# Optimization experiments

Hardware: AMD Instinct MI355X
Metric: run time of the kernel (lower is better)

Reference implementation:

```python
import jax, jax.numpy as jnp
import numpy as np

B, T, N, H = 16, 49, 64, 128  # batch, input_window_size-1, nbones, hidden_size


def setup_inputs() -> dict:
    key = jax.random.key(0)
    ks = jax.random.split(key, 13)
    s = 0.1  # keep gate preactivations in a sane range
    inp = {
        "h": jax.random.normal(ks[0], (B, T, N, H), jnp.float32),
        "c_h": jax.random.normal(ks[1], (B, T, N, H), jnp.float32),
        "p": jax.random.normal(ks[2], (B, T, N, H), jnp.float32),
        "g_t": jax.random.normal(ks[3], (B, T, 1, H), jnp.float32),
        "c_g_t": jax.random.normal(ks[4], (B, T, 1, H), jnp.float32),
        # 8 h-update gates stacked: order = (i, f_lt, f_ft, f_rt, f_s, g, o, c)
        "U": jax.random.normal(ks[5], (8, T, H, H), jnp.float32) * s,     # acts on p
        "Wt": jax.random.normal(ks[6], (8, T, 3 * H, H), jnp.float32) * s,  # acts on [h_before,h,h_after]
        "Ws": jax.random.normal(ks[7], (8, T, H, H), jnp.float32) * s,    # acts on h_s_before
        "Zt": jax.random.normal(ks[8], (8, T, H, H), jnp.float32) * s,    # acts on g_t
        "b": jax.random.normal(ks[9], (8, T, 1, H), jnp.float32) * s,
        # 3 g_t-update gates stacked: order = (forget_f, g, o)
        "Wg": jax.random.normal(ks[10], (3, T, H, H), jnp.float32) * s,
        "Zg": jax.random.normal(ks[11], (3, T, H, H), jnp.float32) * s,
        "bg": jax.random.normal(ks[12], (3, T, 1, H), jnp.float32) * s,
        "train": 0,
    }
    return inp


def _forward(h, c_h, p, g_t, c_g_t, U, Wt, Ws, Zt, b, Wg, Zg, bg):
    zt = jnp.zeros_like(h[:, :1])        # temporal padding [B,1,N,H]
    zs = jnp.zeros_like(h[:, :, :1])     # spatial  padding [B,T,1,H]
    h_tb = jnp.concatenate([zt, h[:, :-1]], axis=1)
    h_ta = jnp.concatenate([h[:, 1:], zt], axis=1)
    h_tba = jnp.concatenate([h_tb, h, h_ta], axis=3)   # [B,T,N,3H]
    c_tb = jnp.concatenate([zt, c_h[:, :-1]], axis=1)
    c_ta = jnp.concatenate([c_h[:, 1:], zt], axis=1)
    h_sb = jnp.concatenate([zs, h[:, :, :-1]], axis=2)
    c_sb = jnp.concatenate([zs, c_h[:, :, :-1]], axis=2)

    # all 8 gate preactivations at once; per-timestep weights contracted with einsum
    pre = (jnp.einsum('btnh,gthk->gbtnk', p, U)
           + jnp.einsum('btnd,gtdk->gbtnk', h_tba, Wt)
           + jnp.einsum('btnh,gthk->gbtnk', h_sb, Ws)
           + jnp.einsum('btoh,gthk->gbtok', g_t, Zt)   # o == 1, broadcasts over bones
           + b[:, None])                               # [8,B,T,N,H]
    i_n, f_lt, f_ft, f_rt, f_s, g_n, o_n = jax.nn.sigmoid(pre[:7])
    c_n = jnp.tanh(pre[7])

    c_h_new = (i_n * c_n + f_lt * c_tb + f_ft * c_h + f_rt * c_ta
               + f_s * c_sb + g_n * c_g_t)
    h_new = o_n * jnp.tanh(c_h_new)

    # global (g_t) state update
    h_mean = jnp.mean(h_new, axis=2, keepdims=True)    # [B,T,1,H]
    f_gtf = jax.nn.sigmoid(jnp.einsum('btnh,thk->btnk', h_new, Wg[0])
                           + jnp.einsum('btoh,thk->btok', g_t, Zg[0]) + bg[0])
    g_gtg = jax.nn.sigmoid(jnp.einsum('btoh,thk->btok', h_mean, Wg[1])
                           + jnp.einsum('btoh,thk->btok', g_t, Zg[1]) + bg[1])
    o_gto = jax.nn.sigmoid(jnp.einsum('btoh,thk->btok', h_mean, Wg[2])
                           + jnp.einsum('btoh,thk->btok', g_t, Zg[2]) + bg[2])
    c_g_new = jnp.mean(f_gtf * c_h_new, axis=2, keepdims=True) + g_gtg * c_g_t
    g_new = jnp.tanh(c_g_new) * o_gto
    return h_new, c_h_new, g_new, c_g_new


def reference(h, c_h, p, g_t, c_g_t, U, Wt, Ws, Zt, b, Wg, Zg, bg, train):
    return _forward(h, c_h, p, g_t, c_g_t, U, Wt, Ws, Zt, b, Wg, Zg, bg)
```

## Files before the change

### kernel.cpp

```cpp
#include <hip/hip_runtime.h>
#include <hip/hip_bf16.h>

#define TD 49
#define BD 16
#define ND 64
#define HD 128

typedef float  f32x4  __attribute__((ext_vector_type(4)));
typedef __bf16 bf16x8 __attribute__((ext_vector_type(8)));
typedef __bf16 bf16x4 __attribute__((ext_vector_type(4)));

#define WP_OFF   0u
#define HB_OFF   32112640u
#define ACT_ELEMS 6422528u
#define PB_OFF   38535168u
#define GB_OFF   44957696u
#define GT_ELEMS 100352u
#define ZP_OFF   45058048u
#define ZB_OFF   45060096u

#define OUT_H    0
#define OUT_CH   6422528
#define OUT_G    12845056
#define OUT_CG   12945408

#define KPAD 136
#define LDS1_BYTES 49152
#define LDS2_BYTES 118784

#define NB_ACTS 12644
#define NB_ZB   392
#define NB_W    1960

__device__ __forceinline__ float sigf(float x) {
    return 1.0f / (1.0f + exp2f(-1.442695041f * x));
}
__device__ __forceinline__ float tanhf_fast(float x) {
    x = fminf(fmaxf(x, -20.f), 20.f);
    float e = exp2f(2.885390082f * x);
    return (e - 1.f) / (e + 1.f);
}
__device__ __forceinline__ void gload16(const void* g, void* l) {
    __builtin_amdgcn_global_load_lds((const __attribute__((address_space(1))) void*)g,
                                     (__attribute__((address_space(3))) void*)l, 16, 0, 0);
}

__global__ __launch_bounds__(256) void prep_kernel(
    const float* __restrict__ h, const float* __restrict__ p,
    const float* __restrict__ g, const float* __restrict__ Zt,
    const float* __restrict__ bias, const float* __restrict__ U,
    const float* __restrict__ Wt, const float* __restrict__ Ws,
    __bf16* __restrict__ ws)
{
    __shared__ float gl[16][128];
    const int bid = blockIdx.x;
    const int tid = threadIdx.x;

    if (bid < NB_ACTS) {
        unsigned i = bid * 256u + tid;
        const unsigned HU = ACT_ELEMS / 4u, GU = GT_ELEMS / 4u;
        const float* src;
        unsigned dst;
        if (i < HU)              { src = h + (size_t)i * 4;            dst = HB_OFF + i * 4; }
        else if (i < 2u*HU)      { unsigned j = i - HU;    src = p + (size_t)j * 4; dst = PB_OFF + j * 4; }
        else if (i < 2u*HU + GU) { unsigned j = i - 2u*HU; src = g + (size_t)j * 4; dst = GB_OFF + j * 4; }
        else if (i < 2u*HU + GU + 512u) {
            unsigned j = i - 2u*HU - GU;
            bf16x4 z = {};
            *(bf16x4*)(ws + ZP_OFF + j * 4) = z;
            return;
        } else return;
        f32x4 v = *(const f32x4*)src;
        bf16x4 w;
        w[0] = (__bf16)v[0]; w[1] = (__bf16)v[1]; w[2] = (__bf16)v[2]; w[3] = (__bf16)v[3];
        *(bf16x4*)(ws + dst) = w;
        return;
    }

    if (bid < NB_ACTS + NB_ZB) {
        int zid = bid - NB_ACTS;
        int t = zid >> 3, gg = zid & 7;
#pragma unroll
        for (int j = 0; j < 8; ++j) {
            int idx = j * 256 + tid;
            int b = idx >> 7, k = idx & 127;
            gl[b][k] = g[((b * TD + t) << 7) + k];
        }
        __syncthreads();

        int h_ = tid & 127, bh = tid >> 7;
        float* zbf = (float*)(ws + ZB_OFF);
        float s[8];
        float bv = bias[(gg * TD + t) * HD + h_];
#pragma unroll
        for (int b8 = 0; b8 < 8; ++b8) s[b8] = bv;
        const float* Zrow = Zt + ((size_t)(gg * TD + t) << 14) + h_;
#pragma unroll 4
        for (int k = 0; k < 128; ++k) {
            float zv = Zrow[k << 7];
#pragma unroll
            for (int b8 = 0; b8 < 8; ++b8)
                s[b8] += gl[bh * 8 + b8][k] * zv;
        }
#pragma unroll
        for (int b8 = 0; b8 < 8; ++b8) {
            int bt = (bh * 8 + b8) * TD + t;
            zbf[(bt * 8 + gg) * HD + h_] = s[b8];
        }
        return;
    }

    {
        int wb = bid - NB_ACTS - NB_ZB;
        int tg = wb / 5, kc = wb % 5;
        int t = tg >> 3, gg = tg & 7;
        int gt = gg * TD + t;
        const float* S;
        int kloc0;
        if (kc == 0)      { S = U  + ((size_t)gt << 14); kloc0 = 0; }
        else if (kc <= 3) { S = Wt + (size_t)gt * 49152; kloc0 = (kc - 1) * 128; }
        else              { S = Ws + ((size_t)gt << 14); kloc0 = 0; }
        __bf16* wrow = ws + WP_OFF + (size_t)tg * 81920 + kc * 128;
#pragma unroll
        for (int u = 0; u < 8; ++u) {
            int gid = u * 256 + tid;
            int hh = gid >> 4, kq = gid & 15;
            const float* s = S + (size_t)(kloc0 + kq * 8) * 128 + hh;
            bf16x8 w;
#pragma unroll
            for (int j = 0; j < 8; ++j) w[j] = (__bf16)s[j * 128];
            *(bf16x8*)(wrow + (size_t)hh * 640 + kq * 8) = w;
        }
    }
}

__global__ __launch_bounds__(256, 3) void phase1_kernel(
    const __bf16* __restrict__ ws,
    const float* __restrict__ c_h, const float* __restrict__ c_g_t,
    float* __restrict__ out)
{
    extern __shared__ __bf16 smem[];
    const __bf16* hb = ws + HB_OFF;
    const __bf16* pb = ws + PB_OFF;
    const __bf16* wp = ws + WP_OFF;
    const __bf16* zp = ws + ZP_OFF;
    const float*  zb = (const float*)(ws + ZB_OFF);

    int bid = blockIdx.x;
    int swz = (bid & 7) * 392 + (bid >> 3);
    int t     = swz >> 6;
    int rem   = swz & 63;
    int mtile = rem >> 3, ntile = rem & 7;

    int tid  = threadIdx.x;
    int wave = tid >> 6, lane = tid & 63;
    int lg = lane >> 4, l16 = lane & 15;

    const __bf16* pA[2][5];
    const __bf16* pB[2];
    int dstA[2], dstB[2];
#pragma unroll
    for (int it = 0; it < 2; ++it) {
        int chunk = it * 256 + tid;
        int row   = chunk >> 2;
        int k16   = chunk & 3;
        int ke    = (k16 ^ ((row >> 1) & 3)) * 8;
        int b_ = mtile * 2 + (row >> 6), n_ = row & 63, bt_ = b_ * TD + t;
        pA[it][0] = pb + ((bt_ * ND + n_) << 7) + ke;
        pA[it][1] = (t > 0)      ? hb + (((bt_ - 1) * ND + n_) << 7) + ke : zp + ke;
        pA[it][2] = hb + ((bt_ * ND + n_) << 7) + ke;
        pA[it][3] = (t < TD - 1) ? hb + (((bt_ + 1) * ND + n_) << 7) + ke : zp + ke;
        pA[it][4] = (n_ > 0)     ? hb + ((bt_ * ND + n_ - 1) << 7) + ke : zp + ke;
        int g_ = row >> 4, hc = row & 15;
        pB[it] = wp + (size_t)((t * 8 + g_) * 128 + ntile * 16 + hc) * 640 + ke;
        dstA[it] = chunk * 8;
        dstB[it] = 12288 + chunk * 8;
    }

    int rbA[2], rbB[8];
#pragma unroll
    for (int mi = 0; mi < 2; ++mi) {
        int row = wave * 32 + mi * 16 + l16;
        rbA[mi] = row * 64 + ((lg ^ ((row >> 1) & 3)) << 4);
    }
#pragma unroll
    for (int g = 0; g < 8; ++g) {
        int row = g * 16 + l16;
        rbB[g] = row * 64 + ((lg ^ ((row >> 1) & 3)) << 4);
    }

    f32x4 acc[2][8];
    const f32x4 vzero = {0.f, 0.f, 0.f, 0.f};
#pragma unroll
    for (int mi = 0; mi < 2; ++mi)
#pragma unroll
        for (int g = 0; g < 8; ++g) acc[mi][g] = vzero;

#define STAGE(KS) do {                                                          \
        const int sl = (KS) % 3;                                                \
        _Pragma("unroll")                                                       \
        for (int it = 0; it < 2; ++it) {                                        \
            gload16(pA[it][(KS) >> 2] + ((KS) & 3) * 32,                        \
                    smem + sl * 4096 + dstA[it]);                               \
            gload16(pB[it] + (KS) * 32,                                         \
                    smem + sl * 4096 + dstB[it]);                               \
        }                                                                       \
    } while (0)

    STAGE(0); STAGE(1);
    asm volatile("s_waitcnt vmcnt(4)" ::: "memory");
    __builtin_amdgcn_s_barrier();

#pragma unroll
    for (int ks = 0; ks < 20; ++ks) {
        if (ks + 2 < 20) STAGE(ks + 2);
        const char* Ab = (const char*)smem + (ks % 3) * 8192;
        const char* Bb = (const char*)smem + 24576 + (ks % 3) * 8192;
        bf16x8 af[2], bfr[8];
        af[0] = *(const bf16x8*)(Ab + rbA[0]);
        af[1] = *(const bf16x8*)(Ab + rbA[1]);
#pragma unroll
        for (int g = 0; g < 8; ++g)
            bfr[g] = *(const bf16x8*)(Bb + rbB[g]);
#pragma unroll
        for (int g = 0; g < 8; ++g) {
            acc[0][g] = __builtin_amdgcn_mfma_f32_16x16x32_bf16(af[0], bfr[g], acc[0][g], 0, 0, 0);
            acc[1][g] = __builtin_amdgcn_mfma_f32_16x16x32_bf16(af[1], bfr[g], acc[1][g], 0, 0, 0);
        }
        if (ks < 19) {
            if (ks + 2 < 20) asm volatile("s_waitcnt vmcnt(4)" ::: "memory");
            else             asm volatile("s_waitcnt vmcnt(0)" ::: "memory");
            __builtin_amdgcn_s_barrier();
        }
    }
#undef STAGE

    const int hcol = ntile * 16 + l16;
#pragma unroll
    for (int mi = 0; mi < 2; ++mi) {
#pragma unroll
        for (int r = 0; r < 4; ++r) {
            int RG = mtile * 128 + wave * 32 + mi * 16 + lg * 4 + r;
            int b  = RG >> 6, nn = RG & 63;
            int bt = b * TD + t;
            int base = ((bt * ND + nn) << 7) + hcol;
            const float* zrow = zb + (bt * 8) * HD + hcol;
            float pre[8];
#pragma unroll
            for (int g = 0; g < 8; ++g) pre[g] = acc[mi][g][r] + zrow[g * HD];
            float i_  = sigf(pre[0]);
            float flt = sigf(pre[1]);
            float fft = sigf(pre[2]);
            float frt = sigf(pre[3]);
            float fs  = sigf(pre[4]);
            float gn  = sigf(pre[5]);
            float on  = sigf(pre[6]);
            float cn  = tanhf_fast(pre[7]);
            float ccur = c_h[base];
            float ctb  = (t > 0)      ? c_h[base - ND * HD] : 0.f;
            float cta  = (t < TD - 1) ? c_h[base + ND * HD] : 0.f;
            float csb  = (nn > 0)     ? c_h[base - HD]      : 0.f;
            float cg   = c_g_t[(bt << 7) + hcol];
            float cnew = i_ * cn + flt * ctb + fft * ccur + frt * cta + fs * csb + gn * cg;
            float hnew = on * tanhf_fast(cnew);
            out[OUT_H  + base] = hnew;
            out[OUT_CH + base] = cnew;
        }
    }
}

__global__ __launch_bounds__(256, 1) void phase2_kernel(
    const float* __restrict__ g_t, const float* __restrict__ c_g_t,
    const float* __restrict__ Wg,  const float* __restrict__ Zg,
    const float* __restrict__ bg,  float* __restrict__ out)
{
    extern __shared__ char sm2[];
    __bf16* A2  = (__bf16*)sm2;
    __bf16* Wb  = (__bf16*)(sm2 + 69632);
    float*  gts = (float*)(sm2 + 69632 + 34816);
    float*  hm  = (float*)(sm2 + 69632 + 34816 + 2048);
    float*  dts = (float*)(sm2 + 69632 + 34816 + 4096);

    int bid = blockIdx.x;
    int t = bid >> 2, bq = bid & 3;
    int tid = threadIdx.x;
    int wv = tid >> 6, lane = tid & 63, lg = lane >> 4, l16 = lane & 15;

    const float* hn  = out + OUT_H;
    const float* chn = out + OUT_CH;

#pragma unroll
    for (int j = 0; j < 32; ++j) {
        int fid = j * 256 + tid;
        int r = fid >> 5, k = (fid & 31) << 2;
        int b = bq * 4 + (r >> 6), nn = r & 63, bt = b * TD + t;
        f32x4 v = *(const f32x4*)(hn + ((bt * ND + nn) << 7) + k);
        bf16x4 w;
        w[0] = (__bf16)v[0]; w[1] = (__bf16)v[1]; w[2] = (__bf16)v[2]; w[3] = (__bf16)v[3];
        *(bf16x4*)(A2 + r * KPAD + k) = w;
    }
#pragma unroll
    for (int j = 0; j < 2; ++j) {
        int idx = j * 256 + tid;
        int b4 = idx >> 7, c = idx & 127;
        gts[idx] = g_t[(((bq * 4 + b4) * TD + t) << 7) + c];
    }
    __syncthreads();

#pragma unroll
    for (int j = 0; j < 2; ++j) {
        int idx = j * 256 + tid;
        int b4 = idx >> 7, c = idx & 127;
        float s = 0.f;
        for (int nn = 0; nn < 64; ++nn) s += (float)A2[(b4 * 64 + nn) * KPAD + c];
        hm[idx] = s * (1.f / 64.f);
    }
    __syncthreads();

    for (int m = 0; m < 5; ++m) {
        const float* M = (m < 3) ? (Zg + ((size_t)(m * TD + t) << 14))
                                 : (Wg + ((size_t)((m - 2) * TD + t) << 14));
#pragma unroll
        for (int j = 0; j < 16; ++j) {
            int fid = j * 256 + tid;
            int k = fid >> 5, c4 = (fid & 31) << 2;
            f32x4 v = *(const f32x4*)(M + (k << 7) + c4);
            bf16x4 w;
            w[0] = (__bf16)v[0]; w[1] = (__bf16)v[1]; w[2] = (__bf16)v[2]; w[3] = (__bf16)v[3];
            *(bf16x4*)(Wb + k * KPAD + c4) = w;
        }
        __syncthreads();
        const float* vec = (m >= 3) ? hm : gts;
#pragma unroll
        for (int j = 0; j < 2; ++j) {
            int idx = j * 256 + tid;
            int b4 = idx >> 7, c = idx & 127;
            float s = 0.f;
            for (int k = 0; k < 128; ++k) s += vec[b4 * 128 + k] * (float)Wb[k * KPAD + c];
            dts[(m * 4 + b4) * 128 + c] = s;
        }
        __syncthreads();
    }

    {
        const float* M = Wg + ((size_t)t << 14);
#pragma unroll
        for (int j = 0; j < 16; ++j) {
            int fid = j * 256 + tid;
            int k = fid >> 5, q = fid & 31;
            f32x4 v = *(const f32x4*)(M + (k << 7) + q * 4);
            int cb = q * 4;
            Wb[(cb + 0) * KPAD + k] = (__bf16)v[0];
            Wb[(cb + 1) * KPAD + k] = (__bf16)v[1];
            Wb[(cb + 2) * KPAD + k] = (__bf16)v[2];
            Wb[(cb + 3) * KPAD + k] = (__bf16)v[3];
        }
        __syncthreads();
    }

    f32x4 acc[4][8];
    const f32x4 vzero = {0.f, 0.f, 0.f, 0.f};
#pragma unroll
    for (int mi = 0; mi < 4; ++mi)
#pragma unroll
        for (int ni = 0; ni < 8; ++ni) acc[mi][ni] = vzero;
#pragma unroll
    for (int ks = 0; ks < 4; ++ks) {
        int kb = ks * 32 + lg * 8;
        bf16x8 a[4];
#pragma unroll
        for (int mi = 0; mi < 4; ++mi)
            a[mi] = *(const bf16x8*)(A2 + (wv * 64 + mi * 16 + l16) * KPAD + kb);
#pragma unroll
        for (int ni = 0; ni < 8; ++ni) {
            bf16x8 bfr = *(const bf16x8*)(Wb + (ni * 16 + l16) * KPAD + kb);
#pragma unroll
            for (int mi = 0; mi < 4; ++mi)
                acc[mi][ni] = __builtin_amdgcn_mfma_f32_16x16x32_bf16(a[mi], bfr, acc[mi][ni], 0, 0, 0);
        }
    }

    int b = bq * 4 + wv, bt = b * TD + t;
#pragma unroll
    for (int ni = 0; ni < 8; ++ni) {
        int col = ni * 16 + l16;
        float z = dts[(0 * 4 + wv) * 128 + col] + bg[t * HD + col];
        float macc = 0.f;
#pragma unroll
        for (int mi = 0; mi < 4; ++mi) {
#pragma unroll
            for (int r = 0; r < 4; ++r) {
                int row = mi * 16 + lg * 4 + r;
                float f  = sigf(acc[mi][ni][r] + z);
                float cv = chn[((bt * ND + row) << 7) + col];
                macc += f * cv;
            }
        }
        macc += __shfl_xor(macc, 16, 64);
        macc += __shfl_xor(macc, 32, 64);
        if (lg == 0) {
            float Mn  = macc * (1.f / 64.f);
            float g_g = sigf(dts[(3 * 4 + wv) * 128 + col] + dts[(1 * 4 + wv) * 128 + col]
                             + bg[(TD + t) * HD + col]);
            float o_g = sigf(dts[(4 * 4 + wv) * 128 + col] + dts[(2 * 4 + wv) * 128 + col]
                             + bg[(2 * TD + t) * HD + col]);
            float cgt = c_g_t[(bt << 7) + col];
            float cgn = Mn + g_g * cgt;
            out[OUT_G  + (bt << 7) + col] = tanhf_fast(cgn) * o_g;
            out[OUT_CG + (bt << 7) + col] = cgn;
        }
    }
}

extern "C" void kernel_launch(void* const* d_in, const int* in_sizes, int n_in,
                              void* d_out, int out_size, void* d_ws, size_t ws_size,
                              hipStream_t stream) {
    const float* h     = (const float*)d_in[0];
    const float* c_h   = (const float*)d_in[1];
    const float* p     = (const float*)d_in[2];
    const float* g_t   = (const float*)d_in[3];
    const float* c_g_t = (const float*)d_in[4];
    const float* U     = (const float*)d_in[5];
    const float* Wt    = (const float*)d_in[6];
    const float* Ws    = (const float*)d_in[7];
    const float* Zt    = (const float*)d_in[8];
    const float* b     = (const float*)d_in[9];
    const float* Wg    = (const float*)d_in[10];
    const float* Zg    = (const float*)d_in[11];
    const float* bg    = (const float*)d_in[12];
    float* out = (float*)d_out;
    __bf16* ws = (__bf16*)d_ws;

    prep_kernel<<<NB_ACTS + NB_ZB + NB_W, 256, 0, stream>>>(h, p, g_t, Zt, b, U, Wt, Ws, ws);

    (void)hipFuncSetAttribute(reinterpret_cast<const void*>(phase1_kernel),
                              hipFuncAttributeMaxDynamicSharedMemorySize, LDS1_BYTES);
    (void)hipFuncSetAttribute(reinterpret_cast<const void*>(phase2_kernel),
                              hipFuncAttributeMaxDynamicSharedMemorySize, LDS2_BYTES);
    phase1_kernel<<<TD * 64, 256, LDS1_BYTES, stream>>>(ws, c_h, c_g_t, out);
    phase2_kernel<<<TD * 4, 256, LDS2_BYTES, stream>>>(g_t, c_g_t, Wg, Zg, bg, out);
}
```

Before: 254.3 us.

## Restructure g_t update: precompute Zg terms, fuse h_mean into phase1, widen phase2 grid

```diff
diff --git a/kernel.cpp b/kernel.cpp
--- a/kernel.cpp
+++ b/kernel.cpp
@@ -18,6 +18,9 @@
 #define GT_ELEMS 100352u
 #define ZP_OFF   45058048u
 #define ZB_OFF   45060096u
+#define HM_OFF   46665728u
+#define DTSG_OFF 46866432u
+#define W0P_OFF  47468544u
 
 #define OUT_H    0
 #define OUT_CH   6422528
@@ -26,11 +29,13 @@
 
 #define KPAD 136
 #define LDS1_BYTES 49152
-#define LDS2_BYTES 118784
+#define LDS2_BYTES 73728
 
 #define NB_ACTS 12644
 #define NB_ZB   392
 #define NB_W    1960
+#define NB_DTSG 147
+#define NB_W0   49
 
 __device__ __forceinline__ float sigf(float x) {
     return 1.0f / (1.0f + exp2f(-1.442695041f * x));
@@ -50,7 +55,8 @@
     const float* __restrict__ g, const float* __restrict__ Zt,
     const float* __restrict__ bias, const float* __restrict__ U,
     const float* __restrict__ Wt, const float* __restrict__ Ws,
-    __bf16* __restrict__ ws)
+    const float* __restrict__ Zg, const float* __restrict__ bg,
+    const float* __restrict__ Wg, __bf16* __restrict__ ws)
 {
     __shared__ float gl[16][128];
     const int bid = blockIdx.x;
@@ -87,7 +93,6 @@
             gl[b][k] = g[((b * TD + t) << 7) + k];
         }
         __syncthreads();
-
         int h_ = tid & 127, bh = tid >> 7;
         float* zbf = (float*)(ws + ZB_OFF);
         float s[8];
@@ -110,7 +115,7 @@
         return;
     }
 
-    {
+    if (bid < NB_ACTS + NB_ZB + NB_W) {
         int wb = bid - NB_ACTS - NB_ZB;
         int tg = wb / 5, kc = wb % 5;
         int t = tg >> 3, gg = tg & 7;
@@ -131,13 +136,62 @@
             for (int j = 0; j < 8; ++j) w[j] = (__bf16)s[j * 128];
             *(bf16x8*)(wrow + (size_t)hh * 640 + kq * 8) = w;
         }
+        return;
+    }
+
+    if (bid < NB_ACTS + NB_ZB + NB_W + NB_DTSG) {
+        int zid = bid - NB_ACTS - NB_ZB - NB_W;
+        int t = zid / 3, m = zid % 3;
+#pragma unroll
+        for (int j = 0; j < 8; ++j) {
+            int idx = j * 256 + tid;
+            int b = idx >> 7, k = idx & 127;
+            gl[b][k] = g[((b * TD + t) << 7) + k];
+        }
+        __syncthreads();
+        int h_ = tid & 127, bh = tid >> 7;
+        float* dtf = (float*)(ws + DTSG_OFF);
+        float s[8];
+        float bv = bg[(m * TD + t) * HD + h_];
+#pragma unroll
+        for (int b8 = 0; b8 < 8; ++b8) s[b8] = bv;
+        const float* Zrow = Zg + ((size_t)(m * TD + t) << 14) + h_;
+#pragma unroll 4
+        for (int k = 0; k < 128; ++k) {
+            float zv = Zrow[k << 7];
+#pragma unroll
+            for (int b8 = 0; b8 < 8; ++b8)
+                s[b8] += gl[bh * 8 + b8][k] * zv;
+        }
+#pragma unroll
+        for (int b8 = 0; b8 < 8; ++b8) {
+            int bt = (bh * 8 + b8) * TD + t;
+            dtf[(m * BD * TD + bt) * HD + h_] = s[b8];
+        }
+        return;
+    }
+
+    {
+        int t = bid - NB_ACTS - NB_ZB - NB_W - NB_DTSG;
+        const float* S = Wg + ((size_t)t << 14);
+        __bf16* dst0 = ws + W0P_OFF + (size_t)t * 16384;
+#pragma unroll
+        for (int u = 0; u < 8; ++u) {
+            int gid = u * 256 + tid;
+            int hh = gid >> 4, kq = gid & 15;
+            const float* s = S + (size_t)(kq * 8) * 128 + hh;
+            bf16x8 w;
+#pragma unroll
+            for (int j = 0; j < 8; ++j) w[j] = (__bf16)s[j * 128];
+            *(bf16x8*)(dst0 + (size_t)hh * 128 + kq * 8) = w;
+        }
     }
 }
 
 __global__ __launch_bounds__(256, 3) void phase1_kernel(
     const __bf16* __restrict__ ws,
     const float* __restrict__ c_h, const float* __restrict__ c_g_t,
-    float* __restrict__ out)
+    float* __restrict__ hmf, float* __restrict__ out)
 {
     extern __shared__ __bf16 smem[];
     const __bf16* hb = ws + HB_OFF;
@@ -236,6 +290,7 @@
 #undef STAGE
 
     const int hcol = ntile * 16 + l16;
+    float s_loc = 0.f;
 #pragma unroll
     for (int mi = 0; mi < 2; ++mi) {
 #pragma unroll
@@ -265,150 +320,132 @@
             float hnew = on * tanhf_fast(cnew);
             out[OUT_H  + base] = hnew;
             out[OUT_CH + base] = cnew;
-        }
-    }
-}
-
-__global__ __launch_bounds__(256, 1) void phase2_kernel(
-    const float* __restrict__ g_t, const float* __restrict__ c_g_t,
-    const float* __restrict__ Wg,  const float* __restrict__ Zg,
-    const float* __restrict__ bg,  float* __restrict__ out)
+            s_loc += hnew;
+        }
+    }
+    s_loc += __shfl_xor(s_loc, 16, 64);
+    s_loc += __shfl_xor(s_loc, 32, 64);
+    __syncthreads();
+    float* redf = (float*)smem;
+    if (lane < 16) redf[wave * 16 + lane] = s_loc;
+    __syncthreads();
+    if (tid < 32) {
+        int bsel = tid >> 4, c = tid & 15;
+        float hv = (redf[(bsel * 2) * 16 + c] + redf[(bsel * 2 + 1) * 16 + c]) * (1.f / 64.f);
+        hmf[((mtile * 2 + bsel) * TD + t) * HD + ntile * 16 + c] = hv;
+    }
+}
+
+__global__ __launch_bounds__(256, 2) void phase2_kernel(
+    const __bf16* __restrict__ ws, const float* __restrict__ c_g_t,
+    const float* __restrict__ Wg, float* __restrict__ out)
 {
     extern __shared__ char sm2[];
     __bf16* A2  = (__bf16*)sm2;
-    __bf16* Wb  = (__bf16*)(sm2 + 69632);
-    float*  gts = (float*)(sm2 + 69632 + 34816);
-    float*  hm  = (float*)(sm2 + 69632 + 34816 + 2048);
-    float*  dts = (float*)(sm2 + 69632 + 34816 + 4096);
+    __bf16* Wb  = (__bf16*)(sm2 + 34816);
+    float*  hm2 = (float*)(sm2 + 69632);
+    float*  red = (float*)(sm2 + 70656);
 
     int bid = blockIdx.x;
-    int t = bid >> 2, bq = bid & 3;
+    int swz = (bid & 7) * 49 + (bid >> 3);
+    int t = swz >> 3, mtile = swz & 7;
     int tid = threadIdx.x;
     int wv = tid >> 6, lane = tid & 63, lg = lane >> 4, l16 = lane & 15;
 
-    const float* hn  = out + OUT_H;
-    const float* chn = out + OUT_CH;
-
-#pragma unroll
-    for (int j = 0; j < 32; ++j) {
+    const float* hn   = out + OUT_H;
+    const float* chn  = out + OUT_CH;
+    const float* hmf  = (const float*)(ws + HM_OFF);
+    const float* dtf  = (const float*)(ws + DTSG_OFF);
+    const __bf16* w0p = ws + W0P_OFF + (size_t)t * 16384;
+
+#pragma unroll
+    for (int j = 0; j < 16; ++j) {
         int fid = j * 256 + tid;
         int r = fid >> 5, k = (fid & 31) << 2;
-        int b = bq * 4 + (r >> 6), nn = r & 63, bt = b * TD + t;
+        int b = mtile * 2 + (r >> 6), nn = r & 63, bt = b * TD + t;
         f32x4 v = *(const f32x4*)(hn + ((bt * ND + nn) << 7) + k);
         bf16x4 w;
         w[0] = (__bf16)v[0]; w[1] = (__bf16)v[1]; w[2] = (__bf16)v[2]; w[3] = (__bf16)v[3];
         *(bf16x4*)(A2 + r * KPAD + k) = w;
     }
 #pragma unroll
-    for (int j = 0; j < 2; ++j) {
+    for (int j = 0; j < 8; ++j) {
         int idx = j * 256 + tid;
-        int b4 = idx >> 7, c = idx & 127;
-        gts[idx] = g_t[(((bq * 4 + b4) * TD + t) << 7) + c];
+        int hh = idx >> 4, kq = idx & 15;
+        bf16x8 v = *(const bf16x8*)(w0p + hh * 128 + kq * 8);
+        *(bf16x8*)(Wb + hh * KPAD + kq * 8) = v;
+    }
+    {
+        int b4 = tid >> 7, c = tid & 127;
+        hm2[b4 * 128 + c] = hmf[((mtile * 2 + b4) * TD + t) * HD + c];
     }
     __syncthreads();
 
-#pragma unroll
-    for (int j = 0; j < 2; ++j) {
-        int idx = j * 256 + tid;
-        int b4 = idx >> 7, c = idx & 127;
-        float s = 0.f;
-        for (int nn = 0; nn < 64; ++nn) s += (float)A2[(b4 * 64 + nn) * KPAD + c];
-        hm[idx] = s * (1.f / 64.f);
-    }
-    __syncthreads();
-
-    for (int m = 0; m < 5; ++m) {
-        const float* M = (m < 3) ? (Zg + ((size_t)(m * TD + t) << 14))
-                                 : (Wg + ((size_t)((m - 2) * TD + t) << 14));
-#pragma unroll
-        for (int j = 0; j < 16; ++j) {
-            int fid = j * 256 + tid;
-            int k = fid >> 5, c4 = (fid & 31) << 2;
-            f32x4 v = *(const f32x4*)(M + (k << 7) + c4);
-            bf16x4 w;
-            w[0] = (__bf16)v[0]; w[1] = (__bf16)v[1]; w[2] = (__bf16)v[2]; w[3] = (__bf16)v[3];
-            *(bf16x4*)(Wb + k * KPAD + c4) = w;
-        }
-        __syncthreads();
-        const float* vec = (m >= 3) ? hm : gts;
-#pragma unroll
-        for (int j = 0; j < 2; ++j) {
-            int idx = j * 256 + tid;
-            int b4 = idx >> 7, c = idx & 127;
-            float s = 0.f;
-            for (int k = 0; k < 128; ++k) s += vec[b4 * 128 + k] * (float)Wb[k * KPAD + c];
-            dts[(m * 4 + b4) * 128 + c] = s;
-        }
-        __syncthreads();
-    }
-
+    float s3 = 0.f, s4 = 0.f;
     {
-        const float* M = Wg + ((size_t)t << 14);
-#pragma unroll
-        for (int j = 0; j < 16; ++j) {
-            int fid = j * 256 + tid;
-            int k = fid >> 5, q = fid & 31;
-            f32x4 v = *(const f32x4*)(M + (k << 7) + q * 4);
-            int cb = q * 4;
-            Wb[(cb + 0) * KPAD + k] = (__bf16)v[0];
-            Wb[(cb + 1) * KPAD + k] = (__bf16)v[1];
-            Wb[(cb + 2) * KPAD + k] = (__bf16)v[2];
-            Wb[(cb + 3) * KPAD + k] = (__bf16)v[3];
-        }
-        __syncthreads();
-    }
-
-    f32x4 acc[4][8];
+        int b4 = tid >> 7, c = tid & 127;
+        const float* W1 = Wg + ((size_t)(TD + t) << 14) + c;
+        const float* W2 = Wg + ((size_t)(2 * TD + t) << 14) + c;
+#pragma unroll 4
+        for (int k = 0; k < 128; ++k) {
+            float hv = hm2[b4 * 128 + k];
+            s3 += hv * W1[k << 7];
+            s4 += hv * W2[k << 7];
+        }
+    }
+
+    f32x4 acc[2][8];
     const f32x4 vzero = {0.f, 0.f, 0.f, 0.f};
 #pragma unroll
-    for (int mi = 0; mi < 4; ++mi)
-#pragma unroll
-        for (int ni = 0; ni < 8; ++ni) acc[mi][ni] = vzero;
+    for (int mi = 0; mi < 2; ++mi)
+#pragma unroll
+        for (int g = 0; g < 8; ++g) acc[mi][g] = vzero;
 #pragma unroll
     for (int ks = 0; ks < 4; ++ks) {
         int kb = ks * 32 + lg * 8;
-        bf16x8 a[4];
-#pragma unroll
-        for (int mi = 0; mi < 4; ++mi)
-            a[mi] = *(const bf16x8*)(A2 + (wv * 64 + mi * 16 + l16) * KPAD + kb);
-#pragma unroll
-        for (int ni = 0; ni < 8; ++ni) {
-            bf16x8 bfr = *(const bf16x8*)(Wb + (ni * 16 + l16) * KPAD + kb);
-#pragma unroll
-            for (int mi = 0; mi < 4; ++mi)
-                acc[mi][ni] = __builtin_amdgcn_mfma_f32_16x16x32_bf16(a[mi], bfr, acc[mi][ni], 0, 0, 0);
-        }
-    }
-
-    int b = bq * 4 + wv, bt = b * TD + t;
-#pragma unroll
-    for (int ni = 0; ni < 8; ++ni) {
-        int col = ni * 16 + l16;
-        float z = dts[(0 * 4 + wv) * 128 + col] + bg[t * HD + col];
+        bf16x8 a0 = *(const bf16x8*)(A2 + (wv * 32 + l16) * KPAD + kb);
+        bf16x8 a1 = *(const bf16x8*)(A2 + (wv * 32 + 16 + l16) * KPAD + kb);
+#pragma unroll
+        for (int g = 0; g < 8; ++g) {
+            bf16x8 bfr = *(const bf16x8*)(Wb + (g * 16 + l16) * KPAD + kb);
+            acc[0][g] = __builtin_amdgcn_mfma_f32_16x16x32_bf16(a0, bfr, acc[0][g], 0, 0, 0);
+            acc[1][g] = __builtin_amdgcn_mfma_f32_16x16x32_bf16(a1, bfr, acc[1][g], 0, 0, 0);
+        }
+    }
+
+    const int bw = mtile * 2 + (wv >> 1);
+    const int btw = bw * TD + t;
+    const float* d0 = dtf + (0 * BD * TD + btw) * HD;
+#pragma unroll
+    for (int cf = 0; cf < 8; ++cf) {
+        int col = cf * 16 + l16;
+        float z = d0[col];
         float macc = 0.f;
 #pragma unroll
-        for (int mi = 0; mi < 4; ++mi) {
+        for (int mi = 0; mi < 2; ++mi) {
 #pragma unroll
             for (int r = 0; r < 4; ++r) {
-                int row = mi * 16 + lg * 4 + r;
-                float f  = sigf(acc[mi][ni][r] + z);
-                float cv = chn[((bt * ND + row) << 7) + col];
+                int row = (wv & 1) * 32 + mi * 16 + lg * 4 + r;
+                float f  = sigf(acc[mi][cf][r] + z);
+                float cv = chn[((btw * ND + row) << 7) + col];
                 macc += f * cv;
             }
         }
         macc += __shfl_xor(macc, 16, 64);
         macc += __shfl_xor(macc, 32, 64);
-        if (lg == 0) {
-            float Mn  = macc * (1.f / 64.f);
-            float g_g = sigf(dts[(3 * 4 + wv) * 128 + col] + dts[(1 * 4 + wv) * 128 + col]
-                             + bg[(TD + t) * HD + col]);
-            float o_g = sigf(dts[(4 * 4 + wv) * 128 + col] + dts[(2 * 4 + wv) * 128 + col]
-                             + bg[(2 * TD + t) * HD + col]);
-            float cgt = c_g_t[(bt << 7) + col];
-            float cgn = Mn + g_g * cgt;
-            out[OUT_G  + (bt << 7) + col] = tanhf_fast(cgn) * o_g;
-            out[OUT_CG + (bt << 7) + col] = cgn;
-        }
+        if (lane < 16) red[wv * 128 + col] = macc;
+    }
+    __syncthreads();
+    {
+        int b4 = tid >> 7, c = tid & 127;
+        int bt = (mtile * 2 + b4) * TD + t;
+        float Mn  = (red[(b4 * 2) * 128 + c] + red[(b4 * 2 + 1) * 128 + c]) * (1.f / 64.f);
+        float g_g = sigf(s3 + dtf[(1 * BD * TD + bt) * HD + c]);
+        float o_g = sigf(s4 + dtf[(2 * BD * TD + bt) * HD + c]);
+        float cgt = c_g_t[(bt << 7) + c];
+        float cgn = Mn + g_g * cgt;
+        out[OUT_G  + (bt << 7) + c] = tanhf_fast(cgn) * o_g;
+        out[OUT_CG + (bt << 7) + c] = cgn;
     }
 }
 
@@ -431,12 +468,14 @@
     float* out = (float*)d_out;
     __bf16* ws = (__bf16*)d_ws;
 
-    prep_kernel<<<NB_ACTS + NB_ZB + NB_W, 256, 0, stream>>>(h, p, g_t, Zt, b, U, Wt, Ws, ws);
+    prep_kernel<<<NB_ACTS + NB_ZB + NB_W + NB_DTSG + NB_W0, 256, 0, stream>>>(
+        h, p, g_t, Zt, b, U, Wt, Ws, Zg, bg, Wg, ws);
 
     (void)hipFuncSetAttribute(reinterpret_cast<const void*>(phase1_kernel),
                               hipFuncAttributeMaxDynamicSharedMemorySize, LDS1_BYTES);
     (void)hipFuncSetAttribute(reinterpret_cast<const void*>(phase2_kernel),
                               hipFuncAttributeMaxDynamicSharedMemorySize, LDS2_BYTES);
-    phase1_kernel<<<TD * 64, 256, LDS1_BYTES, stream>>>(ws, c_h, c_g_t, out);
-    phase2_kernel<<<TD * 4, 256, LDS2_BYTES, stream>>>(g_t, c_g_t, Wg, Zg, bg, out);
-}
+    phase1_kernel<<<TD * 64, 256, LDS1_BYTES, stream>>>(
+        ws, c_h, c_g_t, (float*)(ws + HM_OFF), out);
+    phase2_kernel<<<TD * 8, 256, LDS2_BYTES, stream>>>(ws, c_g_t, Wg, out);
+}
```

Measured after the change: 246.3 us. 1.03x faster.
